# Performance work log

Hardware: AMD Instinct MI355X
Metric: run time of the kernel (lower is better)

## Reference

```python
import jax, jax.numpy as jnp
import numpy as np

N, FIN, FOUT = 4096, 512, 256
ALPHA = 0.2          # LeakyReLU negative slope
NEG_INF = -9e15      # mask value from the torch source


def setup_inputs() -> dict:
    key = jax.random.key(0)
    ks = jax.random.split(key, 11)
    h = jax.random.normal(ks[0], (N, FIN), dtype=jnp.float32)
    adj_n = jax.random.randint(ks[1], (N, N), 0, 2, dtype=jnp.int32)
    adj_d = jax.random.randint(ks[2], (N, N), 0, 2, dtype=jnp.int32)
    G_nd = jax.random.normal(ks[3], (2, N, FOUT), dtype=jnp.float32)
    # learned parameters (xavier-ish scale)
    W_n = jax.random.normal(ks[4], (FIN, FOUT), dtype=jnp.float32) * 0.05
    a1_n = jax.random.normal(ks[5], (FOUT, 1), dtype=jnp.float32) * 0.05
    a2_n = jax.random.normal(ks[6], (FOUT, 1), dtype=jnp.float32) * 0.05
    W_d = jax.random.normal(ks[7], (FIN, FOUT), dtype=jnp.float32) * 0.05
    a1_d = jax.random.normal(ks[8], (FOUT, 1), dtype=jnp.float32) * 0.05
    a2_d = jax.random.normal(ks[9], (FOUT, 1), dtype=jnp.float32) * 0.05
    scale = jnp.zeros((1,), dtype=jnp.float32)
    return {"h": h, "adj_n": adj_n, "adj_d": adj_d, "G_nd": G_nd,
            "W_n": W_n, "a1_n": a1_n, "a2_n": a2_n,
            "W_d": W_d, "a1_d": a1_d, "a2_d": a2_d, "scale": scale}


def _gat(h, adj, W, a1, a2):
    # Wh: [N, FOUT]
    Wh = h @ W
    # outer-sum attention logits: e[i,j] = leakyrelu(Wh_i.a1 + Wh_j.a2)
    e = jax.nn.leaky_relu((Wh @ a1) + (Wh @ a2).T, negative_slope=ALPHA)  # [N, N]
    att = jnp.where(adj > 0, e, jnp.float32(NEG_INF))
    att = jax.nn.softmax(att, axis=-1)
    # dropout is identity in eval mode
    return jax.nn.elu(att @ Wh)  # [N, FOUT]


def reference(h, adj_n, adj_d, G_nd, W_n, a1_n, a2_n, W_d, a1_d, a2_d, scale):
    f_n_S = _gat(h, adj_n, W_n, a1_n, a2_n)
    f_d_S = _gat(h, adj_d, W_d, a1_d, a2_d)
    # The G_nd cross-attention branch (f_nd_C) in the torch source is computed
    # but never used in the returned value; omitted here (jit would DCE it).
    return f_n_S + f_d_S
```

## Files before the change

### kernel.cpp

```cpp
#include <hip/hip_runtime.h>

#define N_NODES 4096
#define FIN     512
#define FOUT    256
#define NSPLIT  4

typedef __attribute__((ext_vector_type(8))) short bf16x8s;
typedef __attribute__((ext_vector_type(4))) float f32x4;
typedef __attribute__((ext_vector_type(8))) unsigned short u16x8;
typedef unsigned short u16;

__device__ inline u16 f2b(float f) {
    union { float f; unsigned int u; } v; v.f = f;
    unsigned int r = v.u + 0x7fffu + ((v.u >> 16) & 1u);
    return (u16)(r >> 16);
}

__global__ __launch_bounds__(256) void prep_kernel(
    const float* __restrict__ h, const float* __restrict__ Wn,
    const float* __restrict__ Wd,
    const float* __restrict__ a1n, const float* __restrict__ a2n,
    const float* __restrict__ a1d, const float* __restrict__ a2d,
    u16* __restrict__ hb, u16* __restrict__ WTb, float* __restrict__ wv)
{
    __shared__ u16 tl[64 * 72];
    __shared__ float sa[256];
    const int t = threadIdx.x;
    const int bid = blockIdx.x;

    if (bid < 1024) {
        int idx = (bid * 256 + t) * 8;
        float4 f0 = *(const float4*)&h[idx];
        float4 f1 = *(const float4*)&h[idx + 4];
        u16x8 o;
        o[0]=f2b(f0.x); o[1]=f2b(f0.y); o[2]=f2b(f0.z); o[3]=f2b(f0.w);
        o[4]=f2b(f1.x); o[5]=f2b(f1.y); o[6]=f2b(f1.z); o[7]=f2b(f1.w);
        *(u16x8*)&hb[idx] = o;
    } else if (bid < 1088) {
        int id = bid - 1024;
        int kx = id & 7, ny = (id >> 3) & 3, b = id >> 5;
        const float* W = b ? Wd : Wn;
        int k0 = kx * 64, n0 = ny * 64;
        int kr = t >> 2, nc0 = (t & 3) * 16;
        const float* src = W + (size_t)(k0 + kr) * FOUT + n0 + nc0;
        #pragma unroll
        for (int jv = 0; jv < 4; ++jv) {
            float4 f = *(const float4*)(src + jv * 4);
            tl[(nc0 + jv * 4 + 0) * 72 + kr] = f2b(f.x);
            tl[(nc0 + jv * 4 + 1) * 72 + kr] = f2b(f.y);
            tl[(nc0 + jv * 4 + 2) * 72 + kr] = f2b(f.z);
            tl[(nc0 + jv * 4 + 3) * 72 + kr] = f2b(f.w);
        }
        __syncthreads();
        int n = t >> 2, kc0 = (t & 3) * 16;
        u16* dst = WTb + ((size_t)b << 17) + (size_t)(n0 + n) * FIN + k0 + kc0;
        *(uint4*)dst       = *(uint4*)&tl[n * 72 + kc0];
        *(uint4*)(dst + 8) = *(uint4*)&tl[n * 72 + kc0 + 8];
    } else {
        int id = bid - 1088;
        int kb = id & 7, v = id >> 3;
        const float* W = (v < 2) ? Wn : Wd;
        const float* a = (v == 0) ? a1n : (v == 1) ? a2n : (v == 2) ? a1d : a2d;
        sa[t] = a[t];
        __syncthreads();
        int k = kb * 64 + (t >> 2);
        int nseg = (t & 3) * 64;
        const float* wr = W + (size_t)k * FOUT + nseg;
        float sum = 0.f;
        #pragma unroll 8
        for (int j = 0; j < 64; ++j) sum += wr[j] * sa[nseg + j];
        sum += __shfl_down(sum, 2, 4);
        sum += __shfl_down(sum, 1, 4);
        if ((t & 3) == 0) wv[v * FIN + k] = sum;
    }
}

__global__ __launch_bounds__(256) void s_kernel(
    const float* __restrict__ h, const float* __restrict__ wv,
    float* __restrict__ s1, float* __restrict__ s2)
{
    const int t = threadIdx.x, lane = t & 63, w = t >> 6;
    const int b = blockIdx.y;
    const int row = blockIdx.x * 4 + w;
    const float* w1 = wv + (b * 2 + 0) * FIN;
    const float* w2 = wv + (b * 2 + 1) * FIN;
    const float* hr = h + (size_t)row * FIN + lane * 8;
    float4 h0 = *(const float4*)hr, h1 = *(const float4*)(hr + 4);
    float4 p0 = *(const float4*)&w1[lane * 8], p1 = *(const float4*)&w1[lane * 8 + 4];
    float4 q0 = *(const float4*)&w2[lane * 8], q1 = *(const float4*)&w2[lane * 8 + 4];
    float d1 = h0.x*p0.x + h0.y*p0.y + h0.z*p0.z + h0.w*p0.w
             + h1.x*p1.x + h1.y*p1.y + h1.z*p1.z + h1.w*p1.w;
    float d2 = h0.x*q0.x + h0.y*q0.y + h0.z*q0.z + h0.w*q0.w
             + h1.x*q1.x + h1.y*q1.y + h1.z*q1.z + h1.w*q1.w;
    #pragma unroll
    for (int off = 32; off >= 1; off >>= 1) {
        d1 += __shfl_xor(d1, off);
        d2 += __shfl_xor(d2, off);
    }
    if (lane == 0) { s1[b * N_NODES + row] = d1; s2[b * N_NODES + row] = d2; }
}

__global__ __launch_bounds__(256) void wh_gemm_kernel(
    const u16* __restrict__ hb, const u16* __restrict__ WTb,
    u16* __restrict__ WhT)
{
    __shared__ u16 smem[8192];
    u16* a_lds = smem;
    u16* b_lds = smem + 4096;

    const int t = threadIdx.x, lane = t & 63, w = t >> 6;
    const int q = lane >> 4, ln = lane & 15;
    const int i0 = blockIdx.x * 64, n0 = blockIdx.y * 64, b = blockIdx.z;
    const u16* wt = WTb + ((size_t)b << 17);

    f32x4 acc[4];
    #pragma unroll
    for (int i = 0; i < 4; ++i) acc[i] = (f32x4){0.f, 0.f, 0.f, 0.f};

    for (int kt = 0; kt < 8; ++kt) {
        const int k0 = kt * 64;
        __syncthreads();
        #pragma unroll
        for (int it = 0; it < 2; ++it) {
            int chunk = it * 256 + t;
            int r = chunk >> 3, kc = chunk & 7;
            const u16* g = hb + (size_t)(i0 + r) * FIN + k0 + ((kc ^ (r & 7)) * 8);
            u16* l = a_lds + (it * 256 + w * 64) * 8;
            __builtin_amdgcn_global_load_lds(
                (const __attribute__((address_space(1))) void*)g,
                (__attribute__((address_space(3))) void*)l, 16, 0, 0);
        }
        #pragma unroll
        for (int it = 0; it < 2; ++it) {
            int chunk = it * 256 + t;
            int n = chunk >> 3, kc = chunk & 7;
            const u16* g = wt + (size_t)(n0 + n) * FIN + k0 + ((kc ^ (n & 7)) * 8);
            u16* l = b_lds + (it * 256 + w * 64) * 8;
            __builtin_amdgcn_global_load_lds(
                (const __attribute__((address_space(1))) void*)g,
                (__attribute__((address_space(3))) void*)l, 16, 0, 0);
        }
        __syncthreads();
        #pragma unroll
        for (int ks = 0; ks < 2; ++ks) {
            int sw = ((ks * 4 + q) ^ (ln & 7)) * 8;
            bf16x8s af = *(const bf16x8s*)&a_lds[(w * 16 + ln) * 64 + sw];
            #pragma unroll
            for (int nt = 0; nt < 4; ++nt) {
                bf16x8s bfv = *(const bf16x8s*)&b_lds[(nt * 16 + ln) * 64 + sw];
                acc[nt] = __builtin_amdgcn_mfma_f32_16x16x32_bf16(af, bfv, acc[nt], 0, 0, 0);
            }
        }
    }
    __syncthreads();
    #pragma unroll
    for (int nt = 0; nt < 4; ++nt)
        #pragma unroll
        for (int r = 0; r < 4; ++r)
            smem[(nt * 16 + ln) * 72 + (w * 16 + q * 4 + r)] = f2b(acc[nt][r]);
    __syncthreads();
    {
        const int nl = t >> 2, is = (t & 3) * 16;
        u16* dst = WhT + ((size_t)b << 20) + (size_t)(n0 + nl) * N_NODES + i0 + is;
        *(uint4*)dst       = *(uint4*)&smem[nl * 72 + is];
        *(uint4*)(dst + 8) = *(uint4*)&smem[nl * 72 + is + 8];
    }
}

__global__ __launch_bounds__(256, 4) void attn_kernel(
    const int* __restrict__ adj_n, const int* __restrict__ adj_d,
    const u16* __restrict__ WhT,
    const float* __restrict__ s1, const float* __restrict__ s2,
    float* __restrict__ num_ws, float* __restrict__ den_ws)
{
    __shared__ u16 wht_lds[256 * 64];
    __shared__ u16 p_lds[32 * 64];
    __shared__ float den_lds[32];

    const int t = threadIdx.x, lane = t & 63, w = t >> 6;
    const int q = lane >> 4, ln = lane & 15;
    const int b = blockIdx.z, split = blockIdx.y;
    const int i0 = blockIdx.x * 32;

    const int* adj = b ? adj_d : adj_n;
    const u16* whtB = WhT + ((size_t)b << 20);
    const float* s1b = s1 + b * N_NODES;
    const float* s2b = s2 + b * N_NODES;

    const int pr = t >> 3;
    const int cw = t & 7;
    const int pc = cw * 8;
    const float s1v = s1b[i0 + pr];
    const size_t adj_row = (size_t)(i0 + pr) * N_NODES + pc;

    if (t < 32) den_lds[t] = 0.f;

    f32x4 acc[2][4];
    #pragma unroll
    for (int mt = 0; mt < 2; ++mt)
        #pragma unroll
        for (int nt = 0; nt < 4; ++nt) acc[mt][nt] = (f32x4){0.f, 0.f, 0.f, 0.f};

    const int jbase = split * (N_NODES / NSPLIT);
    for (int jt = 0; jt < (N_NODES / NSPLIT) / 64; ++jt) {
        const int j0 = jbase + jt * 64;
        __syncthreads();
        int4 av0 = *(const int4*)&adj[adj_row + j0];
        int4 av1 = *(const int4*)&adj[adj_row + j0 + 4];
        float4 sv0 = *(const float4*)&s2b[j0 + pc];
        float4 sv1 = *(const float4*)&s2b[j0 + pc + 4];
        #pragma unroll
        for (int it = 0; it < 8; ++it) {
            int chunk = it * 256 + t;
            int n = chunk >> 3, kc = chunk & 7;
            const u16* g = whtB + (size_t)n * N_NODES + j0 + ((kc ^ (n & 7)) * 8);
            u16* l = wht_lds + (it * 256 + w * 64) * 8;
            __builtin_amdgcn_global_load_lds(
                (const __attribute__((address_space(1))) void*)g,
                (__attribute__((address_space(3))) void*)l, 16, 0, 0);
        }
        int   avi[8] = {av0.x, av0.y, av0.z, av0.w, av1.x, av1.y, av1.z, av1.w};
        float svf[8] = {sv0.x, sv0.y, sv0.z, sv0.w, sv1.x, sv1.y, sv1.z, sv1.w};
        float den_part = 0.f;
        u16x8 pk;
        #pragma unroll
        for (int jj = 0; jj < 8; ++jj) {
            float x = s1v + svf[jj];
            float lr = fmaxf(x, 0.2f * x);
            float p = (avi[jj] > 0) ? __expf(lr) : 0.f;
            den_part += p;
            pk[jj] = f2b(p);
        }
        den_part += __shfl_down(den_part, 4, 8);
        den_part += __shfl_down(den_part, 2, 8);
        den_part += __shfl_down(den_part, 1, 8);
        if ((t & 7) == 0) den_lds[pr] += den_part;
        *(u16x8*)&p_lds[pr * 64 + ((cw ^ (pr & 7)) * 8)] = pk;
        __syncthreads();
        #pragma unroll
        for (int ks = 0; ks < 2; ++ks) {
            int sw = ((ks * 4 + q) ^ (ln & 7)) * 8;
            bf16x8s a0  = *(const bf16x8s*)&p_lds[ln * 64 + sw];
            bf16x8s a1f = *(const bf16x8s*)&p_lds[(16 + ln) * 64 + sw];
            #pragma unroll
            for (int nt = 0; nt < 4; ++nt) {
                bf16x8s bfv = *(const bf16x8s*)&wht_lds[(w * 64 + nt * 16 + ln) * 64 + sw];
                acc[0][nt] = __builtin_amdgcn_mfma_f32_16x16x32_bf16(a0,  bfv, acc[0][nt], 0, 0, 0);
                acc[1][nt] = __builtin_amdgcn_mfma_f32_16x16x32_bf16(a1f, bfv, acc[1][nt], 0, 0, 0);
            }
        }
    }
    const size_t pbase = (size_t)(b * NSPLIT + split) * N_NODES;
    #pragma unroll
    for (int mt = 0; mt < 2; ++mt)
        #pragma unroll
        for (int r = 0; r < 4; ++r) {
            int row = mt * 16 + q * 4 + r;
            #pragma unroll
            for (int nt = 0; nt < 4; ++nt)
                num_ws[(pbase + i0 + row) * FOUT + w * 64 + nt * 16 + ln] = acc[mt][nt][r];
        }
    if (t < 32) den_ws[pbase + i0 + t] = den_lds[t];
}

__global__ __launch_bounds__(256) void reduce_kernel(
    const float* __restrict__ num_ws, const float* __restrict__ den_ws,
    float* __restrict__ out)
{
    int gid = blockIdx.x * 256 + threadIdx.x;
    int i = gid >> 6;
    int f4 = (gid & 63) * 4;
    float4 o = {0.f, 0.f, 0.f, 0.f};
    #pragma unroll
    for (int b = 0; b < 2; ++b) {
        float4 num = {0.f, 0.f, 0.f, 0.f};
        float den = 0.f;
        #pragma unroll
        for (int s = 0; s < NSPLIT; ++s) {
            const float4 v = *(const float4*)&num_ws[((size_t)(b * NSPLIT + s) * N_NODES + i) * FOUT + f4];
            num.x += v.x; num.y += v.y; num.z += v.z; num.w += v.w;
            den += den_ws[(size_t)(b * NSPLIT + s) * N_NODES + i];
        }
        float inv = 1.0f / den;
        float e0 = num.x * inv, e1 = num.y * inv, e2 = num.z * inv, e3 = num.w * inv;
        o.x += (e0 > 0.f) ? e0 : expm1f(e0);
        o.y += (e1 > 0.f) ? e1 : expm1f(e1);
        o.z += (e2 > 0.f) ? e2 : expm1f(e2);
        o.w += (e3 > 0.f) ? e3 : expm1f(e3);
    }
    *(float4*)&out[(size_t)i * FOUT + f4] = o;
}

extern "C" void kernel_launch(void* const* d_in, const int* in_sizes, int n_in,
                              void* d_out, int out_size, void* d_ws, size_t ws_size,
                              hipStream_t stream) {
    const float* h    = (const float*)d_in[0];
    const int*   adjn = (const int*)d_in[1];
    const int*   adjd = (const int*)d_in[2];
    const float* Wn   = (const float*)d_in[4];
    const float* a1n  = (const float*)d_in[5];
    const float* a2n  = (const float*)d_in[6];
    const float* Wd   = (const float*)d_in[7];
    const float* a1d  = (const float*)d_in[8];
    const float* a2d  = (const float*)d_in[9];

    char* ws = (char*)d_ws;
    u16*   hb   = (u16*)ws;
    u16*   WhT  = (u16*)(ws + ((size_t)4 << 20));
    u16*   WTb  = (u16*)(ws + ((size_t)8 << 20));
    float* wv   = (float*)(ws + ((size_t)8 << 20) + (512u << 10));
    float* s1   = wv + 4 * FIN;
    float* s2   = s1 + 2 * N_NODES;
    float* den  = s2 + 2 * N_NODES;
    float* num  = (float*)(ws + ((size_t)9 << 20));

    prep_kernel<<<1120, 256, 0, stream>>>(h, Wn, Wd, a1n, a2n, a1d, a2d, hb, WTb, wv);
    s_kernel<<<dim3(1024, 2), 256, 0, stream>>>(h, wv, s1, s2);
    wh_gemm_kernel<<<dim3(64, 4, 2), 256, 0, stream>>>(hb, WTb, WhT);
    attn_kernel<<<dim3(128, NSPLIT, 2), 256, 0, stream>>>(adjn, adjd, WhT, s1, s2, num, den);
    reduce_kernel<<<1024, 256, 0, stream>>>(num, den, (float*)d_out);
}
```

Before: 223.4 us.

## Bit-pack adjacency in prep and fuse attention scores into GEMM epilogue

The prep kernel now converts both int32 adjacency matrices into 1-bit masks using wavefront ballots. The attention kernel then reads 32x less mask data per tile and prefetches the next tile's mask word and s2 values. The separate s_kernel and the W·a matvec blocks are removed. Instead, s1/s2 are computed in the Wh GEMM epilogue from the accumulators, using shuffles and float atomics into a buffer zeroed by prep, which saves a launch. In exchange, the scores now come from bf16-input GEMM results rather than fp32 dot products, atomic ordering adds nondeterminism, and the full adjacency is still streamed once in prep.

```diff
diff --git a/kernel.cpp b/kernel.cpp
--- a/kernel.cpp
+++ b/kernel.cpp
@@ -4,11 +4,14 @@
 #define FIN     512
 #define FOUT    256
 #define NSPLIT  4
+#define NTILES  ((N_NODES / NSPLIT) / 64)
 
 typedef __attribute__((ext_vector_type(8))) short bf16x8s;
 typedef __attribute__((ext_vector_type(4))) float f32x4;
 typedef __attribute__((ext_vector_type(8))) unsigned short u16x8;
 typedef unsigned short u16;
+typedef unsigned int   u32;
+typedef unsigned long long u64;
 
 __device__ inline u16 f2b(float f) {
     union { float f; unsigned int u; } v; v.f = f;
@@ -19,12 +22,11 @@
 __global__ __launch_bounds__(256) void prep_kernel(
     const float* __restrict__ h, const float* __restrict__ Wn,
     const float* __restrict__ Wd,
-    const float* __restrict__ a1n, const float* __restrict__ a2n,
-    const float* __restrict__ a1d, const float* __restrict__ a2d,
-    u16* __restrict__ hb, u16* __restrict__ WTb, float* __restrict__ wv)
+    const int* __restrict__ adjn, const int* __restrict__ adjd,
+    u16* __restrict__ hb, u16* __restrict__ WTb, u64* __restrict__ bits64,
+    float* __restrict__ s12)
 {
     __shared__ u16 tl[64 * 72];
-    __shared__ float sa[256];
     const int t = threadIdx.x;
     const int bid = blockIdx.x;
 
@@ -36,8 +38,26 @@
         o[0]=f2b(f0.x); o[1]=f2b(f0.y); o[2]=f2b(f0.z); o[3]=f2b(f0.w);
         o[4]=f2b(f1.x); o[5]=f2b(f1.y); o[6]=f2b(f1.z); o[7]=f2b(f1.w);
         *(u16x8*)&hb[idx] = o;
-    } else if (bid < 1088) {
-        int id = bid - 1024;
+    } else if (bid < 2048) {
+        const int lane = t & 63;
+        const long base0 = ((long)(bid - 1024) * 4 + (t >> 6)) * 8192;
+        #pragma unroll 2
+        for (int it = 0; it < 32; ++it) {
+            long base = base0 + (long)it * 256;
+            const int* p = (base < (1L << 24)) ? (adjn + base)
+                                               : (adjd + (base - (1L << 24)));
+            int v0 = p[lane], v1 = p[lane + 64], v2 = p[lane + 128], v3 = p[lane + 192];
+            u64 b0 = __ballot(v0 > 0);
+            u64 b1 = __ballot(v1 > 0);
+            u64 b2 = __ballot(v2 > 0);
+            u64 b3 = __ballot(v3 > 0);
+            if (lane == 0) {
+                u64* d = bits64 + (base >> 6);
+                d[0] = b0; d[1] = b1; d[2] = b2; d[3] = b3;
+            }
+        }
+    } else if (bid < 2112) {
+        int id = bid - 2048;
         int kx = id & 7, ny = (id >> 3) & 3, b = id >> 5;
         const float* W = b ? Wd : Wn;
         int k0 = kx * 64, n0 = ny * 64;
@@ -57,52 +77,18 @@
         *(uint4*)dst       = *(uint4*)&tl[n * 72 + kc0];
         *(uint4*)(dst + 8) = *(uint4*)&tl[n * 72 + kc0 + 8];
     } else {
-        int id = bid - 1088;
-        int kb = id & 7, v = id >> 3;
-        const float* W = (v < 2) ? Wn : Wd;
-        const float* a = (v == 0) ? a1n : (v == 1) ? a2n : (v == 2) ? a1d : a2d;
-        sa[t] = a[t];
-        __syncthreads();
-        int k = kb * 64 + (t >> 2);
-        int nseg = (t & 3) * 64;
-        const float* wr = W + (size_t)k * FOUT + nseg;
-        float sum = 0.f;
-        #pragma unroll 8
-        for (int j = 0; j < 64; ++j) sum += wr[j] * sa[nseg + j];
-        sum += __shfl_down(sum, 2, 4);
-        sum += __shfl_down(sum, 1, 4);
-        if ((t & 3) == 0) wv[v * FIN + k] = sum;
-    }
-}
-
-__global__ __launch_bounds__(256) void s_kernel(
-    const float* __restrict__ h, const float* __restrict__ wv,
-    float* __restrict__ s1, float* __restrict__ s2)
-{
-    const int t = threadIdx.x, lane = t & 63, w = t >> 6;
-    const int b = blockIdx.y;
-    const int row = blockIdx.x * 4 + w;
-    const float* w1 = wv + (b * 2 + 0) * FIN;
-    const float* w2 = wv + (b * 2 + 1) * FIN;
-    const float* hr = h + (size_t)row * FIN + lane * 8;
-    float4 h0 = *(const float4*)hr, h1 = *(const float4*)(hr + 4);
-    float4 p0 = *(const float4*)&w1[lane * 8], p1 = *(const float4*)&w1[lane * 8 + 4];
-    float4 q0 = *(const float4*)&w2[lane * 8], q1 = *(const float4*)&w2[lane * 8 + 4];
-    float d1 = h0.x*p0.x + h0.y*p0.y + h0.z*p0.z + h0.w*p0.w
-             + h1.x*p1.x + h1.y*p1.y + h1.z*p1.z + h1.w*p1.w;
-    float d2 = h0.x*q0.x + h0.y*q0.y + h0.z*q0.z + h0.w*q0.w
-             + h1.x*q1.x + h1.y*q1.y + h1.z*q1.z + h1.w*q1.w;
-    #pragma unroll
-    for (int off = 32; off >= 1; off >>= 1) {
-        d1 += __shfl_xor(d1, off);
-        d2 += __shfl_xor(d2, off);
-    }
-    if (lane == 0) { s1[b * N_NODES + row] = d1; s2[b * N_NODES + row] = d2; }
+        float4 z = {0.f, 0.f, 0.f, 0.f};
+        float4* p4 = (float4*)s12;
+        #pragma unroll
+        for (int k = 0; k < 16; ++k) p4[k * 256 + t] = z;
+    }
 }
 
 __global__ __launch_bounds__(256) void wh_gemm_kernel(
     const u16* __restrict__ hb, const u16* __restrict__ WTb,
-    u16* __restrict__ WhT)
+    const float* __restrict__ a1n, const float* __restrict__ a2n,
+    const float* __restrict__ a1d, const float* __restrict__ a2d,
+    u16* __restrict__ WhT, float* __restrict__ s1, float* __restrict__ s2)
 {
     __shared__ u16 smem[8192];
     u16* a_lds = smem;
@@ -152,6 +138,37 @@
             }
         }
     }
+
+    {
+        const float* a1 = b ? a1d : a1n;
+        const float* a2 = b ? a2d : a2n;
+        float s1p[4] = {0.f, 0.f, 0.f, 0.f};
+        float s2p[4] = {0.f, 0.f, 0.f, 0.f};
+        #pragma unroll
+        for (int nt = 0; nt < 4; ++nt) {
+            float va1 = a1[n0 + nt * 16 + ln];
+            float va2 = a2[n0 + nt * 16 + ln];
+            #pragma unroll
+            for (int r = 0; r < 4; ++r) {
+                s1p[r] += acc[nt][r] * va1;
+                s2p[r] += acc[nt][r] * va2;
+            }
+        }
+        #pragma unroll
+        for (int r = 0; r < 4; ++r) {
+            #pragma unroll
+            for (int off = 8; off >= 1; off >>= 1) {
+                s1p[r] += __shfl_xor(s1p[r], off);
+                s2p[r] += __shfl_xor(s2p[r], off);
+            }
+            if (ln == 0) {
+                int row = i0 + w * 16 + q * 4 + r;
+                atomicAdd(&s1[b * N_NODES + row], s1p[r]);
+                atomicAdd(&s2[b * N_NODES + row], s2p[r]);
+            }
+        }
+    }
+
     __syncthreads();
     #pragma unroll
     for (int nt = 0; nt < 4; ++nt)
@@ -168,7 +185,7 @@
 }
 
 __global__ __launch_bounds__(256, 4) void attn_kernel(
-    const int* __restrict__ adj_n, const int* __restrict__ adj_d,
+    const u32* __restrict__ bits,
     const u16* __restrict__ WhT,
     const float* __restrict__ s1, const float* __restrict__ s2,
     float* __restrict__ num_ws, float* __restrict__ den_ws)
@@ -182,7 +199,6 @@
     const int b = blockIdx.z, split = blockIdx.y;
     const int i0 = blockIdx.x * 32;
 
-    const int* adj = b ? adj_d : adj_n;
     const u16* whtB = WhT + ((size_t)b << 20);
     const float* s1b = s1 + b * N_NODES;
     const float* s2b = s2 + b * N_NODES;
@@ -190,8 +206,10 @@
     const int pr = t >> 3;
     const int cw = t & 7;
     const int pc = cw * 8;
+    const int bsh = (cw & 3) * 8;
     const float s1v = s1b[i0 + pr];
-    const size_t adj_row = (size_t)(i0 + pr) * N_NODES + pc;
+    const u32* bitrow = bits + (size_t)b * (N_NODES * N_NODES / 32)
+                             + (size_t)(i0 + pr) * (N_NODES / 32) + (cw >> 2);
 
     if (t < 32) den_lds[t] = 0.f;
 
@@ -202,13 +220,13 @@
         for (int nt = 0; nt < 4; ++nt) acc[mt][nt] = (f32x4){0.f, 0.f, 0.f, 0.f};
 
     const int jbase = split * (N_NODES / NSPLIT);
-    for (int jt = 0; jt < (N_NODES / NSPLIT) / 64; ++jt) {
+    u32 bw_pf = bitrow[jbase >> 5];
+    float4 sv0_pf = *(const float4*)&s2b[jbase + pc];
+    float4 sv1_pf = *(const float4*)&s2b[jbase + pc + 4];
+
+    for (int jt = 0; jt < NTILES; ++jt) {
         const int j0 = jbase + jt * 64;
         __syncthreads();
-        int4 av0 = *(const int4*)&adj[adj_row + j0];
-        int4 av1 = *(const int4*)&adj[adj_row + j0 + 4];
-        float4 sv0 = *(const float4*)&s2b[j0 + pc];
-        float4 sv1 = *(const float4*)&s2b[j0 + pc + 4];
         #pragma unroll
         for (int it = 0; it < 8; ++it) {
             int chunk = it * 256 + t;
@@ -219,7 +237,14 @@
                 (const __attribute__((address_space(1))) void*)g,
                 (__attribute__((address_space(3))) void*)l, 16, 0, 0);
         }
-        int   avi[8] = {av0.x, av0.y, av0.z, av0.w, av1.x, av1.y, av1.z, av1.w};
+        u32 bw = bw_pf;
+        float4 sv0 = sv0_pf, sv1 = sv1_pf;
+        if (jt < NTILES - 1) {
+            bw_pf = bitrow[(j0 + 64) >> 5];
+            sv0_pf = *(const float4*)&s2b[j0 + 64 + pc];
+            sv1_pf = *(const float4*)&s2b[j0 + 64 + pc + 4];
+        }
+        u32 mask8 = (bw >> bsh) & 0xffu;
         float svf[8] = {sv0.x, sv0.y, sv0.z, sv0.w, sv1.x, sv1.y, sv1.z, sv1.w};
         float den_part = 0.f;
         u16x8 pk;
@@ -227,7 +252,7 @@
         for (int jj = 0; jj < 8; ++jj) {
             float x = s1v + svf[jj];
             float lr = fmaxf(x, 0.2f * x);
-            float p = (avi[jj] > 0) ? __expf(lr) : 0.f;
+            float p = ((mask8 >> jj) & 1u) ? __expf(lr) : 0.f;
             den_part += p;
             pk[jj] = f2b(p);
         }
@@ -305,18 +330,17 @@
     const float* a2d  = (const float*)d_in[9];
 
     char* ws = (char*)d_ws;
-    u16*   hb   = (u16*)ws;
-    u16*   WhT  = (u16*)(ws + ((size_t)4 << 20));
-    u16*   WTb  = (u16*)(ws + ((size_t)8 << 20));
-    float* wv   = (float*)(ws + ((size_t)8 << 20) + (512u << 10));
-    float* s1   = wv + 4 * FIN;
-    float* s2   = s1 + 2 * N_NODES;
-    float* den  = s2 + 2 * N_NODES;
-    float* num  = (float*)(ws + ((size_t)9 << 20));
-
-    prep_kernel<<<1120, 256, 0, stream>>>(h, Wn, Wd, a1n, a2n, a1d, a2d, hb, WTb, wv);
-    s_kernel<<<dim3(1024, 2), 256, 0, stream>>>(h, wv, s1, s2);
-    wh_gemm_kernel<<<dim3(64, 4, 2), 256, 0, stream>>>(hb, WTb, WhT);
-    attn_kernel<<<dim3(128, NSPLIT, 2), 256, 0, stream>>>(adjn, adjd, WhT, s1, s2, num, den);
+    u16*  WhT  = (u16*)ws;
+    u32*  bits = (u32*)(ws + ((size_t)4 << 20));
+    float* s1  = (float*)(ws + ((size_t)8 << 20));
+    float* s2  = s1 + 2 * N_NODES;
+    float* den = s2 + 2 * N_NODES;
+    u16*  hb   = (u16*)(ws + ((size_t)8 << 20) + ((size_t)256 << 10));
+    u16*  WTb  = (u16*)(ws + ((size_t)12 << 20) + ((size_t)256 << 10));
+    float* num = (float*)(ws + ((size_t)8 << 20) + ((size_t)256 << 10));
+
+    prep_kernel<<<2113, 256, 0, stream>>>(h, Wn, Wd, adjn, adjd, hb, WTb, (u64*)bits, s1);
+    wh_gemm_kernel<<<dim3(64, 4, 2), 256, 0, stream>>>(hb, WTb, a1n, a2n, a1d, a2d, WhT, s1, s2);
+    attn_kernel<<<dim3(128, NSPLIT, 2), 256, 0, stream>>>(bits, WhT, s1, s2, num, den);
     reduce_kernel<<<1024, 256, 0, stream>>>(num, den, (float*)d_out);
 }
```

After: 228.3 us. 2.2% more time.
